# Kernel tuning notes

Hardware: AMD Instinct MI355X
Metric: run time of the kernel (lower is better)

The kernel has to match this reference:

```python
import jax, jax.numpy as jnp
import numpy as np

N_NODES = 100000


def gcn_conv(x, src, dst, W, b, n_nodes):
    """PyG GCNConv: out = D^{-1/2} (A + I) D^{-1/2} X W + b (self-loops added)."""
    h = x @ W  # [N, out]
    loops = jnp.arange(n_nodes, dtype=src.dtype)
    s = jnp.concatenate([src, loops])
    d = jnp.concatenate([dst, loops])
    deg = jax.ops.segment_sum(jnp.ones_like(d, dtype=h.dtype), d, num_segments=n_nodes)
    dinv = jnp.where(deg > 0, jax.lax.rsqrt(deg), 0.0)
    norm = dinv[s] * dinv[d]  # [E+N]
    msgs = norm[:, None] * h[s]  # gather + scale
    out = jax.ops.segment_sum(msgs, d, num_segments=n_nodes)
    return out + b


def setup_inputs() -> dict:
    key = jax.random.key(0)
    ks = jax.random.split(key, 10)
    n, e, f_in = N_NODES, 1600000, 128
    x = jax.random.normal(ks[0], (n, f_in), dtype=jnp.float32)
    edge_index = jax.random.randint(ks[1], (2, e), 0, n, dtype=jnp.int64)
    dims = [f_in, 15, 20, 27, 36]
    params = {}
    for i in range(4):
        fan_in, fan_out = dims[i], dims[i + 1]
        scale = 1.0 / np.sqrt(fan_in)
        params[f"W{i+1}"] = jax.random.uniform(ks[2 + 2 * i], (fan_in, fan_out), minval=-scale, maxval=scale, dtype=jnp.float32)
        params[f"b{i+1}"] = jax.random.uniform(ks[3 + 2 * i], (fan_out,), minval=-scale, maxval=scale, dtype=jnp.float32)
    return {"x": x, "edge_index": edge_index, **params}


def reference(x, edge_index, W1, b1, W2, b2, W3, b3, W4, b4):
    src, dst = edge_index[0], edge_index[1]
    n = x.shape[0]
    h = jax.nn.selu(gcn_conv(x, src, dst, W1, b1, n))
    h = jax.nn.selu(gcn_conv(h, src, dst, W2, b2, n))
    h = jax.nn.selu(gcn_conv(h, src, dst, W3, b3, n))
    h = jax.nn.selu(gcn_conv(h, src, dst, W4, b4, n))
    return h
```

## Files before the change

kernel.cpp:

```cpp
#include <hip/hip_runtime.h>
#include <hip/hip_fp16.h>
#include <math.h>

#define BLK 256
#define CBSH 9
#define CBN 512
#define NCBC 256
#define NB2 512

__device__ __forceinline__ float selu_f(float x) {
    const float kScale = 1.0507009873554805f;
    const float kAlpha = 1.6732632423543772f;
    return x > 0.0f ? kScale * x : kScale * kAlpha * expm1f(x);
}

__device__ __forceinline__ float2 h2f2(unsigned u) {
    __half2 h = *reinterpret_cast<__half2*>(&u);
    return __half22float2(h);
}
__device__ __forceinline__ void h8_set(float* a, uint4 v) {
    float2 f0 = h2f2(v.x), f1 = h2f2(v.y), f2 = h2f2(v.z), f3 = h2f2(v.w);
    a[0] = f0.x; a[1] = f0.y; a[2] = f1.x; a[3] = f1.y;
    a[4] = f2.x; a[5] = f2.y; a[6] = f3.x; a[7] = f3.y;
}
__device__ __forceinline__ void h8_add(float* a, uint4 v) {
    float2 f0 = h2f2(v.x), f1 = h2f2(v.y), f2 = h2f2(v.z), f3 = h2f2(v.w);
    a[0] += f0.x; a[1] += f0.y; a[2] += f1.x; a[3] += f1.y;
    a[4] += f2.x; a[5] += f2.y; a[6] += f3.x; a[7] += f3.y;
}
__device__ __forceinline__ uint4 f8_pack(const float* a) {
    __half2 h0 = __float22half2_rn(make_float2(a[0], a[1]));
    __half2 h1 = __float22half2_rn(make_float2(a[2], a[3]));
    __half2 h2 = __float22half2_rn(make_float2(a[4], a[5]));
    __half2 h3 = __float22half2_rn(make_float2(a[6], a[7]));
    uint4 u;
    u.x = *reinterpret_cast<unsigned*>(&h0);
    u.y = *reinterpret_cast<unsigned*>(&h1);
    u.z = *reinterpret_cast<unsigned*>(&h2);
    u.w = *reinterpret_cast<unsigned*>(&h3);
    return u;
}

__global__ void k_cnt(const int* __restrict__ dst, int* __restrict__ H, int e, int nbkt) {
    __shared__ int hist[NCBC];
    int tid = threadIdx.x;
    for (int b = tid; b < nbkt; b += BLK) hist[b] = 0;
    __syncthreads();
    int per = (e + NB2 - 1) / NB2;
    int lo = blockIdx.x * per;
    int hi = min(e, lo + per);
    for (int i = lo + tid; i < hi; i += BLK) atomicAdd(&hist[dst[i] >> CBSH], 1);
    __syncthreads();
    for (int b = tid; b < nbkt; b += BLK) H[blockIdx.x * nbkt + b] = hist[b];
}

__global__ void k_bsum(const int* __restrict__ H, int* __restrict__ bstart, int nbkt, int e) {
    __shared__ int tot[NCBC];
    int tid = threadIdx.x;
    for (int b = tid; b < nbkt; b += BLK) {
        int s = 0;
        for (int i = 0; i < NB2; ++i) s += H[i * nbkt + b];
        tot[b] = s;
    }
    __syncthreads();
    if (tid == 0) {
        int acc = 0;
        for (int b = 0; b < nbkt; ++b) {
            bstart[b] = acc;
            acc += tot[b];
        }
        bstart[nbkt] = acc;
    }
}

__global__ void k_off(int* __restrict__ H, const int* __restrict__ bstart, int nbkt) {
    __shared__ int lds[BLK];
    int b = blockIdx.x, tid = threadIdx.x;
    int v0 = H[(2 * tid) * nbkt + b];
    int v1 = H[(2 * tid + 1) * nbkt + b];
    int pair = v0 + v1;
    lds[tid] = pair;
    __syncthreads();
    int val = pair;
    for (int off = 1; off < BLK; off <<= 1) {
        int t2 = (tid >= off) ? lds[tid - off] : 0;
        __syncthreads();
        val += t2;
        lds[tid] = val;
        __syncthreads();
    }
    int excl = val - pair + bstart[b];
    H[(2 * tid) * nbkt + b] = excl;
    H[(2 * tid + 1) * nbkt + b] = excl + v0;
}

__global__ void k_scatter2(const int* __restrict__ src, const int* __restrict__ dst,
                           const int* __restrict__ H, unsigned* __restrict__ slab,
                           int e, int nbkt) {
    __shared__ int cur[NCBC];
    int tid = threadIdx.x;
    for (int b = tid; b < nbkt; b += BLK) cur[b] = H[blockIdx.x * nbkt + b];
    __syncthreads();
    int per = (e + NB2 - 1) / NB2;
    int lo = blockIdx.x * per;
    int hi = min(e, lo + per);
    for (int i = lo + tid; i < hi; i += BLK) {
        int s = src[i], d = dst[i];
        int b = d >> CBSH;
        int pos = atomicAdd(&cur[b], 1);
        slab[pos] = ((unsigned)s << CBSH) | (unsigned)(d & (CBN - 1));
    }
}

__global__ void k_build(const int* __restrict__ bstart, const unsigned* __restrict__ slab,
                        int* __restrict__ rowptr, float* __restrict__ dinv,
                        int* __restrict__ csr, int n, int e) {
    __shared__ int hist[CBN];
    __shared__ int stmp[BLK];
    int b = blockIdx.x, tid = threadIdx.x;
    hist[2 * tid] = 0;
    hist[2 * tid + 1] = 0;
    __syncthreads();
    int lo = bstart[b], hi = bstart[b + 1];
    for (int i = lo + tid; i < hi; i += BLK) atomicAdd(&hist[slab[i] & (CBN - 1)], 1);
    __syncthreads();
    int h0 = hist[2 * tid], h1 = hist[2 * tid + 1];
    int pair = h0 + h1;
    stmp[tid] = pair;
    __syncthreads();
    int val = pair;
    for (int off = 1; off < BLK; off <<= 1) {
        int t2 = (tid >= off) ? stmp[tid - off] : 0;
        __syncthreads();
        val += t2;
        stmp[tid] = val;
        __syncthreads();
    }
    int e0 = lo + val - pair;
    int e1 = e0 + h0;
    hist[2 * tid] = e0;
    hist[2 * tid + 1] = e1;
    int node0 = b << CBSH;
    int nA = node0 + 2 * tid, nB = nA + 1;
    if (nA < n) { rowptr[nA] = e0; dinv[nA] = rsqrtf((float)(h0 + 1)); }
    if (nB < n) { rowptr[nB] = e1; dinv[nB] = rsqrtf((float)(h1 + 1)); }
    if (b == 0 && tid == 0) rowptr[n] = e;
    __syncthreads();
    for (int i = lo + tid; i < hi; i += BLK) {
        unsigned p = slab[i];
        int pos = atomicAdd(&hist[p & (CBN - 1)], 1);
        csr[pos] = (int)(p >> CBSH);
    }
}

__global__ void k_gemm1(const float* __restrict__ xin, const float* __restrict__ W,
                        const float* __restrict__ dinv, __half* __restrict__ hs, int n) {
    int i = blockIdx.x * BLK + threadIdx.x;
    if (i >= n) return;
    const float* xr = xin + (size_t)i * 128;
    float accf[16];
#pragma unroll
    for (int f = 0; f < 16; ++f) accf[f] = 0.0f;
#pragma unroll
    for (int k4 = 0; k4 < 32; ++k4) {
        float4 xv = *reinterpret_cast<const float4*>(xr + k4 * 4);
        float xs4[4] = {xv.x, xv.y, xv.z, xv.w};
#pragma unroll
        for (int j = 0; j < 4; ++j) {
            const int k = k4 * 4 + j;
#pragma unroll
            for (int f = 0; f < 15; ++f) accf[f] = fmaf(xs4[j], W[k * 15 + f], accf[f]);
        }
    }
    float di = dinv[i];
#pragma unroll
    for (int f = 0; f < 15; ++f) accf[f] *= di;
    accf[15] = 0.0f;
    __half2* ro2 = reinterpret_cast<__half2*>(hs + (size_t)i * 16);
#pragma unroll
    for (int f2 = 0; f2 < 8; ++f2)
        ro2[f2] = __float22half2_rn(make_float2(accf[2 * f2], accf[2 * f2 + 1]));
}

template <int CHI, int NPN, int SIN, int K, int FN, int CHO, int SON>
__global__ void k_aggemm(const int* __restrict__ rowptr, const int* __restrict__ csr,
                         const __half* __restrict__ hsin, const float* __restrict__ bprev,
                         const float* __restrict__ dinv, const float* __restrict__ W,
                         __half* __restrict__ hsout, int n) {
    int lane = threadIdx.x & 63;
    int g = lane / CHI;
    int fl = lane - g * CHI;
    int wid = (blockIdx.x * BLK + threadIdx.x) >> 6;
    int d = wid * NPN + g;
    bool active = (g < NPN) && (d < n);
    float xv8[8];
#pragma unroll
    for (int j = 0; j < 8; ++j) xv8[j] = 0.0f;
    float di = 0.0f;
    if (active) {
        di = dinv[d];
        int beg = rowptr[d], end = rowptr[d + 1];
        auto rowp = [&](int r) {
            return reinterpret_cast<const uint4*>(hsin + (size_t)r * SIN) + fl;
        };
        float s0[8], s1[8] = {0}, s2[8] = {0}, s3[8] = {0};
        h8_set(s0, *rowp(d));
        int p = beg;
        for (; p + 8 <= end; p += 8) {
            int e0 = __builtin_nontemporal_load(csr + p);
            int e1 = __builtin_nontemporal_load(csr + p + 1);
            int e2 = __builtin_nontemporal_load(csr + p + 2);
            int e3 = __builtin_nontemporal_load(csr + p + 3);
            int e4 = __builtin_nontemporal_load(csr + p + 4);
            int e5 = __builtin_nontemporal_load(csr + p + 5);
            int e6 = __builtin_nontemporal_load(csr + p + 6);
            int e7 = __builtin_nontemporal_load(csr + p + 7);
            uint4 v0 = *rowp(e0), v1 = *rowp(e1), v2 = *rowp(e2), v3 = *rowp(e3);
            uint4 v4 = *rowp(e4), v5 = *rowp(e5), v6 = *rowp(e6), v7 = *rowp(e7);
            h8_add(s0, v0); h8_add(s1, v1); h8_add(s2, v2); h8_add(s3, v3);
            h8_add(s0, v4); h8_add(s1, v5); h8_add(s2, v6); h8_add(s3, v7);
        }
        for (; p + 4 <= end; p += 4) {
            int e0 = __builtin_nontemporal_load(csr + p);
            int e1 = __builtin_nontemporal_load(csr + p + 1);
            int e2 = __builtin_nontemporal_load(csr + p + 2);
            int e3 = __builtin_nontemporal_load(csr + p + 3);
            uint4 v0 = *rowp(e0), v1 = *rowp(e1), v2 = *rowp(e2), v3 = *rowp(e3);
            h8_add(s0, v0); h8_add(s1, v1); h8_add(s2, v2); h8_add(s3, v3);
        }
        for (; p < end; ++p) h8_add(s0, *rowp(__builtin_nontemporal_load(csr + p)));
#pragma unroll
        for (int j = 0; j < 8; ++j) {
            int k = fl * 8 + j;
            if (k < K) {
                float s = (s0[j] + s1[j]) + (s2[j] + s3[j]);
                xv8[j] = selu_f(di * s + bprev[k]);
            }
        }
    }
    int base = lane - fl;
    float xk[K];
#pragma unroll
    for (int k = 0; k < K; ++k)
        xk[k] = __shfl(xv8[k & 7], (base + (k >> 3)) & 63, 64);
    if (active) {
#pragma unroll
        for (int m = 0; m < (CHO + CHI - 1) / CHI; ++m) {
            int c = fl + m * CHI;
            if (c < CHO) {
                float acc[8];
#pragma unroll
                for (int j = 0; j < 8; ++j) acc[j] = 0.0f;
#pragma unroll
                for (int k = 0; k < K; ++k) {
#pragma unroll
                    for (int j = 0; j < 8; ++j) {
                        int col = c * 8 + j;
                        if (col < FN) acc[j] = fmaf(xk[k], W[k * FN + col], acc[j]);
                    }
                }
                float gg[8];
#pragma unroll
                for (int j = 0; j < 8; ++j) {
                    int col = c * 8 + j;
                    gg[j] = (col < FN) ? di * acc[j] : 0.0f;
                }
                *reinterpret_cast<uint4*>(hsout + (size_t)d * SON + c * 8) = f8_pack(gg);
            }
        }
    }
}

template <int F, int S, int ACT, int NPN>
__global__ void k_aggL(const int* __restrict__ rowptr, const int* __restrict__ csr,
                       const __half* __restrict__ hs, float* __restrict__ out,
                       const float* __restrict__ dinv, const float* __restrict__ bias,
                       int n) {
    int lane = threadIdx.x & 63;
    int g = lane / ACT;
    int fl = lane - g * ACT;
    int wid = (blockIdx.x * BLK + threadIdx.x) >> 6;
    int d = wid * NPN + g;
    if (g >= NPN || d >= n) return;
    int beg = rowptr[d], end = rowptr[d + 1];
    auto rowp = [&](int r) {
        return reinterpret_cast<const uint4*>(hs + (size_t)r * S) + fl;
    };
    float s0[8], s1[8] = {0}, s2[8] = {0}, s3[8] = {0};
    h8_set(s0, *rowp(d));
    int p = beg;
    for (; p + 8 <= end; p += 8) {
        int e0 = __builtin_nontemporal_load(csr + p);
        int e1 = __builtin_nontemporal_load(csr + p + 1);
        int e2 = __builtin_nontemporal_load(csr + p + 2);
        int e3 = __builtin_nontemporal_load(csr + p + 3);
        int e4 = __builtin_nontemporal_load(csr + p + 4);
        int e5 = __builtin_nontemporal_load(csr + p + 5);
        int e6 = __builtin_nontemporal_load(csr + p + 6);
        int e7 = __builtin_nontemporal_load(csr + p + 7);
        uint4 v0 = *rowp(e0), v1 = *rowp(e1), v2 = *rowp(e2), v3 = *rowp(e3);
        uint4 v4 = *rowp(e4), v5 = *rowp(e5), v6 = *rowp(e6), v7 = *rowp(e7);
        h8_add(s0, v0); h8_add(s1, v1); h8_add(s2, v2); h8_add(s3, v3);
        h8_add(s0, v4); h8_add(s1, v5); h8_add(s2, v6); h8_add(s3, v7);
    }
    for (; p + 4 <= end; p += 4) {
        int e0 = __builtin_nontemporal_load(csr + p);
        int e1 = __builtin_nontemporal_load(csr + p + 1);
        int e2 = __builtin_nontemporal_load(csr + p + 2);
        int e3 = __builtin_nontemporal_load(csr + p + 3);
        uint4 v0 = *rowp(e0), v1 = *rowp(e1), v2 = *rowp(e2), v3 = *rowp(e3);
        h8_add(s0, v0); h8_add(s1, v1); h8_add(s2, v2); h8_add(s3, v3);
    }
    for (; p < end; ++p) h8_add(s0, *rowp(__builtin_nontemporal_load(csr + p)));
    float dv = dinv[d];
    float r[8];
#pragma unroll
    for (int j = 0; j < 8; ++j) {
        int col = fl * 8 + j;
        float s = (s0[j] + s1[j]) + (s2[j] + s3[j]);
        r[j] = (col < F) ? selu_f(dv * s + bias[col]) : 0.0f;
    }
    float* op = out + (size_t)d * F + fl * 8;
    *reinterpret_cast<float4*>(op) = make_float4(r[0], r[1], r[2], r[3]);
    if (fl * 8 + 4 < F)
        *reinterpret_cast<float4*>(op + 4) = make_float4(r[4], r[5], r[6], r[7]);
}

extern "C" void kernel_launch(void* const* d_in, const int* in_sizes, int n_in,
                              void* d_out, int out_size, void* d_ws, size_t ws_size,
                              hipStream_t stream) {
    const float* x = (const float*)d_in[0];
    const int* ei = (const int*)d_in[1];
    const float* W1 = (const float*)d_in[2];
    const float* b1 = (const float*)d_in[3];
    const float* W2 = (const float*)d_in[4];
    const float* b2 = (const float*)d_in[5];
    const float* W3 = (const float*)d_in[6];
    const float* b3 = (const float*)d_in[7];
    const float* W4 = (const float*)d_in[8];
    const float* b4 = (const float*)d_in[9];

    int n = in_sizes[0] / 128;
    int e = in_sizes[1] / 2;
    const int* s32 = ei;
    const int* d32 = ei + e;
    int nbkt = (n + CBN - 1) >> CBSH;

    char* w = (char*)d_ws;
    auto alloc = [&](size_t bytes) {
        char* p = w;
        w += (bytes + 255) & ~(size_t)255;
        return p;
    };
    int* rowptr = (int*)alloc(((size_t)n + 1) * 4);
    float* dinv = (float*)alloc((size_t)n * 4);
    int* csr = (int*)alloc((size_t)e * 4);
    int* H = (int*)alloc((size_t)NB2 * nbkt * 4);
    int* bstart = (int*)alloc(((size_t)nbkt + 1) * 4);
    __half* bufA = (__half*)alloc((size_t)n * 40 * 2);
    __half* bufC = (__half*)alloc((size_t)n * 40 * 2);
    unsigned* slab = (unsigned*)bufA;

    int nb = (n + BLK - 1) / BLK;

    k_cnt<<<NB2, BLK, 0, stream>>>(d32, H, e, nbkt);
    k_bsum<<<1, BLK, 0, stream>>>(H, bstart, nbkt, e);
    k_off<<<nbkt, BLK, 0, stream>>>(H, bstart, nbkt);
    k_scatter2<<<NB2, BLK, 0, stream>>>(s32, d32, H, slab, e, nbkt);
    k_build<<<nbkt, BLK, 0, stream>>>(bstart, slab, rowptr, dinv, csr, n, e);

    int ab1 = (n + 127) / 128;
    int ab2 = (n + 83) / 84;
    int ab3 = (n + 63) / 64;
    int ab4 = (n + 47) / 48;

    k_gemm1<<<nb, BLK, 0, stream>>>(x, W1, dinv, bufA, n);

    k_aggemm<2, 32, 16, 15, 20, 3, 32><<<ab1, BLK, 0, stream>>>(
        rowptr, csr, bufA, b1, dinv, W2, bufC, n);

    k_aggemm<3, 21, 32, 20, 27, 4, 32><<<ab2, BLK, 0, stream>>>(
        rowptr, csr, bufC, b2, dinv, W3, bufA, n);

    k_aggemm<4, 16, 32, 27, 36, 5, 40><<<ab3, BLK, 0, stream>>>(
        rowptr, csr, bufA, b3, dinv, W4, bufC, n);

    k_aggL<36, 40, 5, 12><<<ab4, BLK, 0, stream>>>(rowptr, csr, bufC, (float*)d_out, dinv, b4, n);
}
```

Before: 249.4 us.

## Split each node's neighbor gather across two lane groups and combine via shuffle

Each destination node's edge list is now split in half, with two lane groups gathering the halves in parallel and combining the partial sums through a warp shuffle. The number of nodes per wavefront is halved and grid sizes double to match. The aim is to raise memory-level parallelism and shorten per-node latency chains in the gather-bound aggregation. In exchange the inner loop drops from 8-wide to 4-wide unrolling and there are extra shuffles and more wavefronts.

```diff
diff --git a/kernel.cpp b/kernel.cpp
--- a/kernel.cpp
+++ b/kernel.cpp
@@ -17,11 +17,6 @@
 __device__ __forceinline__ float2 h2f2(unsigned u) {
     __half2 h = *reinterpret_cast<__half2*>(&u);
     return __half22float2(h);
-}
-__device__ __forceinline__ void h8_set(float* a, uint4 v) {
-    float2 f0 = h2f2(v.x), f1 = h2f2(v.y), f2 = h2f2(v.z), f3 = h2f2(v.w);
-    a[0] = f0.x; a[1] = f0.y; a[2] = f1.x; a[3] = f1.y;
-    a[4] = f2.x; a[5] = f2.y; a[6] = f3.x; a[7] = f3.y;
 }
 __device__ __forceinline__ void h8_add(float* a, uint4 v) {
     float2 f0 = h2f2(v.x), f1 = h2f2(v.y), f2 = h2f2(v.z), f3 = h2f2(v.w);
@@ -182,128 +177,22 @@
         ro2[f2] = __float22half2_rn(make_float2(accf[2 * f2], accf[2 * f2 + 1]));
 }
 
-template <int CHI, int NPN, int SIN, int K, int FN, int CHO, int SON>
-__global__ void k_aggemm(const int* __restrict__ rowptr, const int* __restrict__ csr,
-                         const __half* __restrict__ hsin, const float* __restrict__ bprev,
-                         const float* __restrict__ dinv, const float* __restrict__ W,
-                         __half* __restrict__ hsout, int n) {
-    int lane = threadIdx.x & 63;
-    int g = lane / CHI;
-    int fl = lane - g * CHI;
-    int wid = (blockIdx.x * BLK + threadIdx.x) >> 6;
-    int d = wid * NPN + g;
-    bool active = (g < NPN) && (d < n);
-    float xv8[8];
-#pragma unroll
-    for (int j = 0; j < 8; ++j) xv8[j] = 0.0f;
-    float di = 0.0f;
-    if (active) {
-        di = dinv[d];
-        int beg = rowptr[d], end = rowptr[d + 1];
-        auto rowp = [&](int r) {
-            return reinterpret_cast<const uint4*>(hsin + (size_t)r * SIN) + fl;
-        };
-        float s0[8], s1[8] = {0}, s2[8] = {0}, s3[8] = {0};
-        h8_set(s0, *rowp(d));
-        int p = beg;
-        for (; p + 8 <= end; p += 8) {
-            int e0 = __builtin_nontemporal_load(csr + p);
-            int e1 = __builtin_nontemporal_load(csr + p + 1);
-            int e2 = __builtin_nontemporal_load(csr + p + 2);
-            int e3 = __builtin_nontemporal_load(csr + p + 3);
-            int e4 = __builtin_nontemporal_load(csr + p + 4);
-            int e5 = __builtin_nontemporal_load(csr + p + 5);
-            int e6 = __builtin_nontemporal_load(csr + p + 6);
-            int e7 = __builtin_nontemporal_load(csr + p + 7);
-            uint4 v0 = *rowp(e0), v1 = *rowp(e1), v2 = *rowp(e2), v3 = *rowp(e3);
-            uint4 v4 = *rowp(e4), v5 = *rowp(e5), v6 = *rowp(e6), v7 = *rowp(e7);
-            h8_add(s0, v0); h8_add(s1, v1); h8_add(s2, v2); h8_add(s3, v3);
-            h8_add(s0, v4); h8_add(s1, v5); h8_add(s2, v6); h8_add(s3, v7);
-        }
-        for (; p + 4 <= end; p += 4) {
-            int e0 = __builtin_nontemporal_load(csr + p);
-            int e1 = __builtin_nontemporal_load(csr + p + 1);
-            int e2 = __builtin_nontemporal_load(csr + p + 2);
-            int e3 = __builtin_nontemporal_load(csr + p + 3);
-            uint4 v0 = *rowp(e0), v1 = *rowp(e1), v2 = *rowp(e2), v3 = *rowp(e3);
-            h8_add(s0, v0); h8_add(s1, v1); h8_add(s2, v2); h8_add(s3, v3);
-        }
-        for (; p < end; ++p) h8_add(s0, *rowp(__builtin_nontemporal_load(csr + p)));
-#pragma unroll
-        for (int j = 0; j < 8; ++j) {
-            int k = fl * 8 + j;
-            if (k < K) {
-                float s = (s0[j] + s1[j]) + (s2[j] + s3[j]);
-                xv8[j] = selu_f(di * s + bprev[k]);
-            }
-        }
-    }
-    int base = lane - fl;
-    float xk[K];
-#pragma unroll
-    for (int k = 0; k < K; ++k)
-        xk[k] = __shfl(xv8[k & 7], (base + (k >> 3)) & 63, 64);
-    if (active) {
-#pragma unroll
-        for (int m = 0; m < (CHO + CHI - 1) / CHI; ++m) {
-            int c = fl + m * CHI;
-            if (c < CHO) {
-                float acc[8];
-#pragma unroll
-                for (int j = 0; j < 8; ++j) acc[j] = 0.0f;
-#pragma unroll
-                for (int k = 0; k < K; ++k) {
-#pragma unroll
-                    for (int j = 0; j < 8; ++j) {
-                        int col = c * 8 + j;
-                        if (col < FN) acc[j] = fmaf(xk[k], W[k * FN + col], acc[j]);
-                    }
-                }
-                float gg[8];
-#pragma unroll
-                for (int j = 0; j < 8; ++j) {
-                    int col = c * 8 + j;
-                    gg[j] = (col < FN) ? di * acc[j] : 0.0f;
-                }
-                *reinterpret_cast<uint4*>(hsout + (size_t)d * SON + c * 8) = f8_pack(gg);
-            }
-        }
-    }
-}
-
-template <int F, int S, int ACT, int NPN>
-__global__ void k_aggL(const int* __restrict__ rowptr, const int* __restrict__ csr,
-                       const __half* __restrict__ hs, float* __restrict__ out,
-                       const float* __restrict__ dinv, const float* __restrict__ bias,
-                       int n) {
-    int lane = threadIdx.x & 63;
-    int g = lane / ACT;
-    int fl = lane - g * ACT;
-    int wid = (blockIdx.x * BLK + threadIdx.x) >> 6;
-    int d = wid * NPN + g;
-    if (g >= NPN || d >= n) return;
+template <int CHI, int SIN>
+__device__ __forceinline__ void gather_half(const int* __restrict__ rowptr,
+                                            const int* __restrict__ csr,
+                                            const __half* __restrict__ hsin,
+                                            int d, int fl, int half, float* s ) {
     int beg = rowptr[d], end = rowptr[d + 1];
+    int mid = beg + ((end - beg) >> 1);
+    int myb = half ? mid : beg;
+    int mye = half ? end : mid;
     auto rowp = [&](int r) {
-        return reinterpret_cast<const uint4*>(hs + (size_t)r * S) + fl;
+        return reinterpret_cast<const uint4*>(hsin + (size_t)r * SIN) + fl;
     };
-    float s0[8], s1[8] = {0}, s2[8] = {0}, s3[8] = {0};
-    h8_set(s0, *rowp(d));
-    int p = beg;
-    for (; p + 8 <= end; p += 8) {
-        int e0 = __builtin_nontemporal_load(csr + p);
-        int e1 = __builtin_nontemporal_load(csr + p + 1);
-        int e2 = __builtin_nontemporal_load(csr + p + 2);
-        int e3 = __builtin_nontemporal_load(csr + p + 3);
-        int e4 = __builtin_nontemporal_load(csr + p + 4);
-        int e5 = __builtin_nontemporal_load(csr + p + 5);
-        int e6 = __builtin_nontemporal_load(csr + p + 6);
-        int e7 = __builtin_nontemporal_load(csr + p + 7);
-        uint4 v0 = *rowp(e0), v1 = *rowp(e1), v2 = *rowp(e2), v3 = *rowp(e3);
-        uint4 v4 = *rowp(e4), v5 = *rowp(e5), v6 = *rowp(e6), v7 = *rowp(e7);
-        h8_add(s0, v0); h8_add(s1, v1); h8_add(s2, v2); h8_add(s3, v3);
-        h8_add(s0, v4); h8_add(s1, v5); h8_add(s2, v6); h8_add(s3, v7);
-    }
-    for (; p + 4 <= end; p += 4) {
+    float s0[8] = {0}, s1[8] = {0}, s2[8] = {0}, s3[8] = {0};
+    if (!half) h8_add(s0, *rowp(d));
+    int p = myb;
+    for (; p + 4 <= mye; p += 4) {
         int e0 = __builtin_nontemporal_load(csr + p);
         int e1 = __builtin_nontemporal_load(csr + p + 1);
         int e2 = __builtin_nontemporal_load(csr + p + 2);
@@ -311,19 +200,108 @@
         uint4 v0 = *rowp(e0), v1 = *rowp(e1), v2 = *rowp(e2), v3 = *rowp(e3);
         h8_add(s0, v0); h8_add(s1, v1); h8_add(s2, v2); h8_add(s3, v3);
     }
-    for (; p < end; ++p) h8_add(s0, *rowp(__builtin_nontemporal_load(csr + p)));
-    float dv = dinv[d];
-    float r[8];
+    for (; p < mye; ++p) h8_add(s0, *rowp(__builtin_nontemporal_load(csr + p)));
+#pragma unroll
+    for (int j = 0; j < 8; ++j) s[j] = (s0[j] + s1[j]) + (s2[j] + s3[j]);
+}
+
+template <int CHI, int NPN, int SIN, int K, int FN, int CHO, int SON>
+__global__ void k_aggemm(const int* __restrict__ rowptr, const int* __restrict__ csr,
+                         const __half* __restrict__ hsin, const float* __restrict__ bprev,
+                         const float* __restrict__ dinv, const float* __restrict__ W,
+                         __half* __restrict__ hsout, int n) {
+    constexpr int LPN = 2 * CHI;
+    int lane = threadIdx.x & 63;
+    int g = lane / LPN;
+    int r = lane - g * LPN;
+    int half = r / CHI;
+    int fl = r - half * CHI;
+    int wid = (blockIdx.x * BLK + threadIdx.x) >> 6;
+    int d = wid * NPN + g;
+    bool active = (g < NPN) && (d < n);
+    float part[8];
+#pragma unroll
+    for (int j = 0; j < 8; ++j) part[j] = 0.0f;
+    float di = 0.0f;
+    if (active) {
+        di = dinv[d];
+        gather_half<CHI, SIN>(rowptr, csr, hsin, d, fl, half, part);
+    }
+    int partner = lane + (half ? -CHI : CHI);
+    float xv8[8];
 #pragma unroll
     for (int j = 0; j < 8; ++j) {
-        int col = fl * 8 + j;
-        float s = (s0[j] + s1[j]) + (s2[j] + s3[j]);
-        r[j] = (col < F) ? selu_f(dv * s + bias[col]) : 0.0f;
-    }
-    float* op = out + (size_t)d * F + fl * 8;
-    *reinterpret_cast<float4*>(op) = make_float4(r[0], r[1], r[2], r[3]);
-    if (fl * 8 + 4 < F)
-        *reinterpret_cast<float4*>(op + 4) = make_float4(r[4], r[5], r[6], r[7]);
+        float t = __shfl(part[j], partner & 63, 64);
+        float s = part[j] + t;
+        int k = fl * 8 + j;
+        xv8[j] = (k < K) ? selu_f(di * s + bprev[k]) : 0.0f;
+    }
+    int base = lane - r;
+    float xk[K];
+#pragma unroll
+    for (int k = 0; k < K; ++k)
+        xk[k] = __shfl(xv8[k & 7], (base + (k >> 3)) & 63, 64);
+    if (active && r < CHO) {
+        int c = r;
+        float acc[8];
+#pragma unroll
+        for (int j = 0; j < 8; ++j) acc[j] = 0.0f;
+#pragma unroll
+        for (int k = 0; k < K; ++k) {
+#pragma unroll
+            for (int j = 0; j < 8; ++j) {
+                int col = c * 8 + j;
+                if (col < FN) acc[j] = fmaf(xk[k], W[k * FN + col], acc[j]);
+            }
+        }
+        float gg[8];
+#pragma unroll
+        for (int j = 0; j < 8; ++j) {
+            int col = c * 8 + j;
+            gg[j] = (col < FN) ? di * acc[j] : 0.0f;
+        }
+        *reinterpret_cast<uint4*>(hsout + (size_t)d * SON + c * 8) = f8_pack(gg);
+    }
+}
+
+template <int F, int S, int ACT, int NPN>
+__global__ void k_aggL(const int* __restrict__ rowptr, const int* __restrict__ csr,
+                       const __half* __restrict__ hs, float* __restrict__ out,
+                       const float* __restrict__ dinv, const float* __restrict__ bias,
+                       int n) {
+    constexpr int LPN = 2 * ACT;
+    int lane = threadIdx.x & 63;
+    int g = lane / LPN;
+    int r = lane - g * LPN;
+    int half = r / ACT;
+    int fl = r - half * ACT;
+    int wid = (blockIdx.x * BLK + threadIdx.x) >> 6;
+    int d = wid * NPN + g;
+    bool active = (g < NPN) && (d < n);
+    float part[8];
+#pragma unroll
+    for (int j = 0; j < 8; ++j) part[j] = 0.0f;
+    if (active) gather_half<ACT, S>(rowptr, csr, hs, d, fl, half, part);
+    int partner = lane + (half ? -ACT : ACT);
+    float sum[8];
+#pragma unroll
+    for (int j = 0; j < 8; ++j) {
+        float t = __shfl(part[j], partner & 63, 64);
+        sum[j] = part[j] + t;
+    }
+    if (active && half == 0) {
+        float dv = dinv[d];
+        float rr[8];
+#pragma unroll
+        for (int j = 0; j < 8; ++j) {
+            int col = fl * 8 + j;
+            rr[j] = (col < F) ? selu_f(dv * sum[j] + bias[col]) : 0.0f;
+        }
+        float* op = out + (size_t)d * F + fl * 8;
+        *reinterpret_cast<float4*>(op) = make_float4(rr[0], rr[1], rr[2], rr[3]);
+        if (fl * 8 + 4 < F)
+            *reinterpret_cast<float4*>(op + 4) = make_float4(rr[4], rr[5], rr[6], rr[7]);
+    }
 }
 
 extern "C" void kernel_launch(void* const* d_in, const int* in_sizes, int n_in,
@@ -369,21 +347,21 @@
     k_scatter2<<<NB2, BLK, 0, stream>>>(s32, d32, H, slab, e, nbkt);
     k_build<<<nbkt, BLK, 0, stream>>>(bstart, slab, rowptr, dinv, csr, n, e);
 
-    int ab1 = (n + 127) / 128;
-    int ab2 = (n + 83) / 84;
-    int ab3 = (n + 63) / 64;
-    int ab4 = (n + 47) / 48;
+    int ab1 = (n + 63) / 64;
+    int ab2 = (n + 39) / 40;
+    int ab3 = (n + 31) / 32;
+    int ab4 = (n + 23) / 24;
 
     k_gemm1<<<nb, BLK, 0, stream>>>(x, W1, dinv, bufA, n);
 
-    k_aggemm<2, 32, 16, 15, 20, 3, 32><<<ab1, BLK, 0, stream>>>(
+    k_aggemm<2, 16, 16, 15, 20, 3, 32><<<ab1, BLK, 0, stream>>>(
         rowptr, csr, bufA, b1, dinv, W2, bufC, n);
 
-    k_aggemm<3, 21, 32, 20, 27, 4, 32><<<ab2, BLK, 0, stream>>>(
+    k_aggemm<3, 10, 32, 20, 27, 4, 32><<<ab2, BLK, 0, stream>>>(
         rowptr, csr, bufC, b2, dinv, W3, bufA, n);
 
-    k_aggemm<4, 16, 32, 27, 36, 5, 40><<<ab3, BLK, 0, stream>>>(
+    k_aggemm<4, 8, 32, 27, 36, 5, 40><<<ab3, BLK, 0, stream>>>(
         rowptr, csr, bufA, b3, dinv, W4, bufC, n);
 
-    k_aggL<36, 40, 5, 12><<<ab4, BLK, 0, stream>>>(rowptr, csr, bufC, (float*)d_out, dinv, b4, n);
-}
+    k_aggL<36, 40, 5, 6><<<ab4, BLK, 0, stream>>>(rowptr, csr, bufC, (float*)d_out, dinv, b4, n);
+}
```

Result: slower. 324.4 us (+30.1%).
